# Performance work log

Hardware: AMD Instinct MI355X
Metric: run time of the kernel (lower is better)

Reference implementation:

```python
import jax, jax.numpy as jnp
import numpy as np

WAYS, SHOTS = 5, 5
F_DIM, HID = 1024, 512          # num_node_feats, int(1024*0.5)
BATCH = 2048                    # num_tasks
N = WAYS * SHOTS + 1            # 26 samples per episode
BN_EPS = 1e-5


def setup_inputs() -> dict:
    key = jax.random.key(0)
    ks = jax.random.split(key, 12)
    d = {"node_feats": jax.random.normal(ks[0], (BATCH, N, F_DIM), jnp.float32)}
    # conv1 (1x1): F_DIM -> HID, bn1; conv2: HID -> HID, bn2; conv4: HID -> F_DIM
    d["w1"] = jax.random.normal(ks[1], (HID, F_DIM), jnp.float32) * (1.0 / np.sqrt(F_DIM))
    d["b1"] = jax.random.normal(ks[2], (HID,), jnp.float32) * 0.01
    d["g1"] = jnp.ones((HID,), jnp.float32)
    d["be1"] = jnp.zeros((HID,), jnp.float32)
    d["m1"] = jax.random.normal(ks[3], (HID,), jnp.float32) * 0.1
    d["v1"] = jax.random.uniform(ks[4], (HID,), jnp.float32, 0.5, 1.5)
    d["w2"] = jax.random.normal(ks[5], (HID, HID), jnp.float32) * (1.0 / np.sqrt(HID))
    d["b2"] = jax.random.normal(ks[6], (HID,), jnp.float32) * 0.01
    d["g2"] = jnp.ones((HID,), jnp.float32)
    d["be2"] = jnp.zeros((HID,), jnp.float32)
    d["m2"] = jax.random.normal(ks[7], (HID,), jnp.float32) * 0.1
    d["v2"] = jax.random.uniform(ks[8], (HID,), jnp.float32, 0.5, 1.5)
    d["w3"] = jax.random.normal(ks[9], (F_DIM, HID), jnp.float32) * (1.0 / np.sqrt(HID))
    d["b3"] = jax.random.normal(ks[10], (F_DIM,), jnp.float32) * 0.01
    return d


def _conv1x1(x, w, b):
    # x: [B, Cin, N], w: [Cout, Cin] -> [B, Cout, N]
    return jnp.einsum('bcn,oc->bon', x, w) + b[None, :, None]


def _bn(x, g, be, m, v):
    # inference BatchNorm1d over channel dim of [B, C, N]
    scale = g / jnp.sqrt(v + BN_EPS)
    return (x - m[None, :, None]) * scale[None, :, None] + be[None, :, None]


def _forward(node_feats, w1, b1, g1, be1, m1, v1, w2, b2, g2, be2, m2, v2, w3, b3):
    B, n, F = node_feats.shape  # n == WAYS*SHOTS+1
    # in-place per-class mean on the transpose view also mutates node_feats in torch:
    sup = node_feats[:, :WAYS * SHOTS].reshape(B, WAYS, SHOTS, F)
    sup = jnp.broadcast_to(sup.mean(axis=2, keepdims=True), sup.shape).reshape(B, WAYS * SHOTS, F)
    nf = jnp.concatenate([sup, node_feats[:, WAYS * SHOTS:]], axis=1)  # [B, N, F]

    x = nf.transpose(0, 2, 1)  # [B, F, N]
    x = jax.nn.leaky_relu(_bn(_conv1x1(x, w1, b1), g1, be1, m1, v1), 0.01)
    x = jax.nn.leaky_relu(_bn(_conv1x1(x, w2, b2), g2, be2, m2, v2), 0.01)
    att = jax.nn.sigmoid(_conv1x1(x, w3, b3))  # [B, F, N]

    # sim_cal: cosine sim of u_ij = a_i*a_j*x_i vs v_ij = a_i*a_j*x_j, fused into matmuls.
    a = att.transpose(0, 2, 1)       # [B, N, F]
    a2 = a * a                       # attention squared
    P = a2 * nf                      # dot(u,v)   = (P P^T)[i,j]
    Q = a2 * nf * nf                 # ||u_ij||^2 = (Q a2^T)[i,j]
    dots = jnp.einsum('bif,bjf->bij', P, P)    # [B, N, N]
    n2 = jnp.einsum('bif,bjf->bij', Q, a2)     # [B, N, N]
    nrm = jnp.sqrt(n2)
    sim = dots / (nrm * nrm.transpose(0, 2, 1))
    pred = jnp.stack([sim, 1.0 - sim], axis=1)  # [B, 2, N, N]
    return jnp.clip(pred, 0.0, 1.0)


def reference(node_feats, w1, b1, g1, be1, m1, v1, w2, b2, g2, be2, m2, v2, w3, b3):
    return _forward(node_feats, w1, b1, g1, be1, m1, v1, w2, b2, g2, be2, m2, v2, w3, b3)
```

## Files before the change

kernel.cpp:

```cpp
#include <hip/hip_runtime.h>
#include <hip/hip_bf16.h>
#include <math.h>

typedef __bf16 bf16_t;
typedef bf16_t bf16x8 __attribute__((ext_vector_type(8)));
typedef float f32x4 __attribute__((ext_vector_type(4)));

#define WAYS 5
#define SHOTS 5
#define F_DIM 1024
#define HID 512
#define BATCH 2048
#define NN 26
#define NC 6
#define MROWS (BATCH * NC)

#define S1 (HID * F_DIM)
#define S2 (HID * HID)
#define S3 (F_DIM * HID)

#define TM 48
#define PADX 520

__global__ __launch_bounds__(256)
void cvt_all_kernel(const float* __restrict__ w1, const float* __restrict__ w2,
                    const float* __restrict__ w3, bf16_t* __restrict__ out) {
    int i = (blockIdx.x * 256 + threadIdx.x) * 4;
    if (i >= S1 + S2 + S3) return;
    const float* src;
    int j = i;
    if (i < S1)            { src = w1; }
    else if (i < S1 + S2)  { src = w2; j = i - S1; }
    else                   { src = w3; j = i - S1 - S2; }
    float4 v = *(const float4*)(src + j);
    out[i + 0] = (bf16_t)v.x;
    out[i + 1] = (bf16_t)v.y;
    out[i + 2] = (bf16_t)v.z;
    out[i + 3] = (bf16_t)v.w;
}

__global__ __launch_bounds__(128)
void nfc_kernel(const float* __restrict__ node, bf16_t* __restrict__ nfc_b) {
    int row = blockIdx.x;
    int b = row / NC;
    int w = row - b * NC;
    int f = threadIdx.x * 8;
    const float* src = node + (size_t)b * NN * F_DIM;
    float acc[8];
    if (w < WAYS) {
        #pragma unroll
        for (int e = 0; e < 8; ++e) acc[e] = 0.f;
        #pragma unroll
        for (int s = 0; s < SHOTS; ++s) {
            const float* r = src + (size_t)(w * SHOTS + s) * F_DIM + f;
            float4 v0 = *(const float4*)r;
            float4 v1 = *(const float4*)(r + 4);
            acc[0] += v0.x; acc[1] += v0.y; acc[2] += v0.z; acc[3] += v0.w;
            acc[4] += v1.x; acc[5] += v1.y; acc[6] += v1.z; acc[7] += v1.w;
        }
        #pragma unroll
        for (int e = 0; e < 8; ++e) acc[e] *= 0.2f;
    } else {
        const float* r = src + (size_t)25 * F_DIM + f;
        float4 v0 = *(const float4*)r;
        float4 v1 = *(const float4*)(r + 4);
        acc[0] = v0.x; acc[1] = v0.y; acc[2] = v0.z; acc[3] = v0.w;
        acc[4] = v1.x; acc[5] = v1.y; acc[6] = v1.z; acc[7] = v1.w;
    }
    bf16x8 ob;
    #pragma unroll
    for (int e = 0; e < 8; ++e) ob[e] = (bf16_t)acc[e];
    *(bf16x8*)(nfc_b + (size_t)row * F_DIM + f) = ob;
}

__global__ __launch_bounds__(256)
void fused_mlp(const bf16_t* __restrict__ nfc, const bf16_t* __restrict__ w1b,
               const bf16_t* __restrict__ w2b, const bf16_t* __restrict__ w3b,
               bf16_t* __restrict__ att,
               const float* __restrict__ b1, const float* __restrict__ g1,
               const float* __restrict__ be1, const float* __restrict__ m1,
               const float* __restrict__ v1,
               const float* __restrict__ b2, const float* __restrict__ g2,
               const float* __restrict__ be2, const float* __restrict__ m2,
               const float* __restrict__ v2,
               const float* __restrict__ b3) {
    __shared__ bf16_t X1[TM * PADX];
    __shared__ bf16_t X2[TM * PADX];
    const int tid = threadIdx.x;
    const int lane = tid & 63;
    const int wv = tid >> 6;
    const int l15 = lane & 15, quad = lane >> 4;
    const int bm = blockIdx.x * TM;
    const int nb = wv * 128;

    f32x4 acc[3][8];

    auto mmac = [&](bf16x8 (&af)[6], bf16x8 (&bf)[16]) {
        #pragma unroll
        for (int kk = 0; kk < 2; ++kk)
            #pragma unroll
            for (int mt = 0; mt < 3; ++mt)
                #pragma unroll
                for (int nt = 0; nt < 8; ++nt)
                    acc[mt][nt] = __builtin_amdgcn_mfma_f32_16x16x32_bf16(
                        af[mt * 2 + kk], bf[nt * 2 + kk], acc[mt][nt], 0, 0, 0);
    };
    auto ldB = [&](bf16x8 (&bf)[16], const bf16_t* W, int K, int c) {
        #pragma unroll
        for (int nt = 0; nt < 8; ++nt)
            #pragma unroll
            for (int kk = 0; kk < 2; ++kk)
                bf[nt * 2 + kk] = *(const bf16x8*)(W + (size_t)(nb + nt * 16 + l15) * K
                                                   + c * 64 + kk * 32 + quad * 8);
    };
    auto ldA1 = [&](bf16x8 (&af)[6], int c) {
        #pragma unroll
        for (int mt = 0; mt < 3; ++mt)
            #pragma unroll
            for (int kk = 0; kk < 2; ++kk)
                af[mt * 2 + kk] = *(const bf16x8*)(nfc + (size_t)(bm + mt * 16 + l15) * F_DIM
                                                    + c * 64 + kk * 32 + quad * 8);
    };
    auto ldAx = [&](bf16x8 (&af)[6], int which, int c) {
        #pragma unroll
        for (int mt = 0; mt < 3; ++mt)
            #pragma unroll
            for (int kk = 0; kk < 2; ++kk) {
                int idx = (mt * 16 + l15) * PADX + c * 64 + kk * 32 + quad * 8;
                af[mt * 2 + kk] = which ? *(const bf16x8*)&X2[idx] : *(const bf16x8*)&X1[idx];
            }
    };

    bf16x8 aF0[6], aF1[6], bF0[16], bF1[16];

    #pragma unroll
    for (int mt = 0; mt < 3; ++mt)
        #pragma unroll
        for (int nt = 0; nt < 8; ++nt)
            acc[mt][nt] = (f32x4){0.f, 0.f, 0.f, 0.f};
    ldA1(aF0, 0); ldB(bF0, w1b, F_DIM, 0);
    for (int c = 0; c < 16; c += 2) {
        ldA1(aF1, c + 1); ldB(bF1, w1b, F_DIM, c + 1);
        mmac(aF0, bF0);
        if (c + 2 < 16) { ldA1(aF0, c + 2); ldB(bF0, w1b, F_DIM, c + 2); }
        mmac(aF1, bF1);
    }
    #pragma unroll
    for (int nt = 0; nt < 8; ++nt) {
        const int n = nb + nt * 16 + l15;
        const float sg = g1[n] * rsqrtf(v1[n] + 1e-5f);
        const float tt = (b1[n] - m1[n]) * sg + be1[n];
        #pragma unroll
        for (int mt = 0; mt < 3; ++mt) {
            const int row = mt * 16 + quad * 4;
            #pragma unroll
            for (int r = 0; r < 4; ++r) {
                float y = acc[mt][nt][r] * sg + tt;
                y = y > 0.f ? y : 0.01f * y;
                X1[(row + r) * PADX + n] = (bf16_t)y;
            }
        }
    }
    __syncthreads();

    #pragma unroll
    for (int mt = 0; mt < 3; ++mt)
        #pragma unroll
        for (int nt = 0; nt < 8; ++nt)
            acc[mt][nt] = (f32x4){0.f, 0.f, 0.f, 0.f};
    ldB(bF0, w2b, HID, 0);
    for (int c = 0; c < 8; c += 2) {
        ldB(bF1, w2b, HID, c + 1);
        ldAx(aF0, 0, c);
        mmac(aF0, bF0);
        if (c + 2 < 8) ldB(bF0, w2b, HID, c + 2);
        ldAx(aF1, 0, c + 1);
        mmac(aF1, bF1);
    }
    #pragma unroll
    for (int nt = 0; nt < 8; ++nt) {
        const int n = nb + nt * 16 + l15;
        const float sg = g2[n] * rsqrtf(v2[n] + 1e-5f);
        const float tt = (b2[n] - m2[n]) * sg + be2[n];
        #pragma unroll
        for (int mt = 0; mt < 3; ++mt) {
            const int row = mt * 16 + quad * 4;
            #pragma unroll
            for (int r = 0; r < 4; ++r) {
                float y = acc[mt][nt][r] * sg + tt;
                y = y > 0.f ? y : 0.01f * y;
                X2[(row + r) * PADX + n] = (bf16_t)y;
            }
        }
    }
    __syncthreads();

    #pragma unroll
    for (int h = 0; h < 2; ++h) {
        const bf16_t* w3h = w3b + (size_t)(h * 512) * HID;
        #pragma unroll
        for (int mt = 0; mt < 3; ++mt)
            #pragma unroll
            for (int nt = 0; nt < 8; ++nt)
                acc[mt][nt] = (f32x4){0.f, 0.f, 0.f, 0.f};
        ldB(bF0, w3h, HID, 0);
        for (int c = 0; c < 8; c += 2) {
            ldB(bF1, w3h, HID, c + 1);
            ldAx(aF0, 1, c);
            mmac(aF0, bF0);
            if (c + 2 < 8) ldB(bF0, w3h, HID, c + 2);
            ldAx(aF1, 1, c + 1);
            mmac(aF1, bF1);
        }
        #pragma unroll
        for (int nt = 0; nt < 8; ++nt) {
            const int n = h * 512 + nb + nt * 16 + l15;
            const float tt = b3[n];
            #pragma unroll
            for (int mt = 0; mt < 3; ++mt) {
                const int m = bm + mt * 16 + quad * 4;
                #pragma unroll
                for (int r = 0; r < 4; ++r) {
                    float y = acc[mt][nt][r] + tt;
                    y = 1.0f / (1.0f + __expf(-y));
                    att[(size_t)(m + r) * F_DIM + n] = (bf16_t)y;
                }
            }
        }
    }
}

__global__ __launch_bounds__(256)
void sim_kernel(const bf16_t* __restrict__ nfc, const bf16_t* __restrict__ att,
                float* __restrict__ out) {
    __shared__ float sx[NC * F_DIM];
    __shared__ float sa[NC * F_DIM];
    __shared__ float dmat[NC * NC], n2mat[NC * NC], simc[NC * NC];
    const int b = blockIdx.x, tid = threadIdx.x;
    const bf16_t* xs = nfc + (size_t)b * NC * F_DIM;
    const bf16_t* as = att + (size_t)b * NC * F_DIM;
    for (int i = tid * 8; i < NC * F_DIM; i += 256 * 8) {
        bf16x8 vx = *(const bf16x8*)&xs[i];
        bf16x8 va = *(const bf16x8*)&as[i];
        #pragma unroll
        for (int e = 0; e < 8; ++e) { sx[i + e] = (float)vx[e]; sa[i + e] = (float)va[e]; }
    }
    __syncthreads();
    const int lane = tid & 63, wid = tid >> 6;
    const int ti[21] = {0,0,0,0,0,0,1,1,1,1,1,2,2,2,2,3,3,3,4,4,5};
    const int tj[21] = {0,1,2,3,4,5,1,2,3,4,5,2,3,4,5,3,4,5,4,5,5};
    for (int t = wid; t < 21; t += 4) {
        const int i = ti[t], j = tj[t];
        float d = 0.f, qij = 0.f, qji = 0.f;
        for (int f = lane; f < F_DIM; f += 64) {
            float ai = sa[i * F_DIM + f], aj = sa[j * F_DIM + f];
            float xi = sx[i * F_DIM + f], xj = sx[j * F_DIM + f];
            float a2i = ai * ai, a2j = aj * aj;
            float pi = a2i * xi, pj = a2j * xj;
            d   += pi * pj;
            qij += pi * xi * a2j;
            qji += pj * xj * a2i;
        }
        #pragma unroll
        for (int off = 32; off > 0; off >>= 1) {
            d   += __shfl_xor(d, off);
            qij += __shfl_xor(qij, off);
            qji += __shfl_xor(qji, off);
        }
        if (lane == 0) {
            dmat[i * NC + j] = d; dmat[j * NC + i] = d;
            n2mat[i * NC + j] = qij; n2mat[j * NC + i] = qji;
        }
    }
    __syncthreads();
    if (tid < NC * NC) {
        int i = tid / NC, j = tid - (tid / NC) * NC;
        simc[tid] = dmat[tid] / sqrtf(n2mat[i * NC + j] * n2mat[j * NC + i]);
    }
    __syncthreads();
    float* o = out + (size_t)b * (2 * NN * NN);
    for (int e = tid; e < 2 * NN * NN; e += 256) {
        int ch = e / (NN * NN);
        int rem = e - ch * (NN * NN);
        int i = rem / NN, j = rem - (rem / NN) * NN;
        float s = simc[(i / 5) * NC + (j / 5)];
        float v = ch ? 1.0f - s : s;
        v = fminf(fmaxf(v, 0.0f), 1.0f);
        o[e] = v;
    }
}

extern "C" void kernel_launch(void* const* d_in, const int* in_sizes, int n_in,
                              void* d_out, int out_size, void* d_ws, size_t ws_size,
                              hipStream_t stream) {
    const float* node = (const float*)d_in[0];
    const float* w1  = (const float*)d_in[1];
    const float* b1  = (const float*)d_in[2];
    const float* g1  = (const float*)d_in[3];
    const float* be1 = (const float*)d_in[4];
    const float* m1  = (const float*)d_in[5];
    const float* v1  = (const float*)d_in[6];
    const float* w2  = (const float*)d_in[7];
    const float* b2  = (const float*)d_in[8];
    const float* g2  = (const float*)d_in[9];
    const float* be2 = (const float*)d_in[10];
    const float* m2  = (const float*)d_in[11];
    const float* v2  = (const float*)d_in[12];
    const float* w3  = (const float*)d_in[13];
    const float* b3  = (const float*)d_in[14];
    float* out = (float*)d_out;

    char* ws = (char*)d_ws;
    size_t off = 0;
    bf16_t* wall  = (bf16_t*)(ws + off); off += (size_t)(S1 + S2 + S3) * 2;
    bf16_t* w1b = wall, *w2b = wall + S1, *w3b = wall + S1 + S2;
    bf16_t* nfc_b = (bf16_t*)(ws + off); off += (size_t)MROWS * F_DIM * 2;
    bf16_t* attb  = (bf16_t*)(ws + off); off += (size_t)MROWS * F_DIM * 2;

    cvt_all_kernel<<<((S1 + S2 + S3) / 4 + 255) / 256, 256, 0, stream>>>(w1, w2, w3, wall);
    nfc_kernel<<<MROWS, 128, 0, stream>>>(node, nfc_b);
    fused_mlp<<<MROWS / TM, 256, 0, stream>>>(nfc_b, w1b, w2b, w3b, attb,
                                              b1, g1, be1, m1, v1,
                                              b2, g2, be2, m2, v2, b3);
    sim_kernel<<<BATCH, 256, 0, stream>>>(nfc_b, attb, out);
}
```

Baseline: 468.4 us.

## Split fused MLP across eight waves with smaller per-wave N tiles

Doubles the fused_mlp block from 256 to 512 threads, so each of eight waves covers 64 output columns instead of 128. This halves the accumulator and B-fragment registers per wave and adds a launch-bounds hint of two blocks per CU, aiming for more resident waves to hide memory latency. It also software-pipelines the LDS A-fragment loads in layers 2 and 3 alongside the B loads. In exchange, each W row is fetched by twice as many waves relative to the MFMA work, and the 2x~50KB LDS footprint may limit how many blocks actually fit.

```diff
diff --git a/kernel.cpp b/kernel.cpp
--- a/kernel.cpp
+++ b/kernel.cpp
@@ -73,7 +73,7 @@
     *(bf16x8*)(nfc_b + (size_t)row * F_DIM + f) = ob;
 }
 
-__global__ __launch_bounds__(256)
+__global__ __launch_bounds__(512, 2)
 void fused_mlp(const bf16_t* __restrict__ nfc, const bf16_t* __restrict__ w1b,
                const bf16_t* __restrict__ w2b, const bf16_t* __restrict__ w3b,
                bf16_t* __restrict__ att,
@@ -91,23 +91,30 @@
     const int wv = tid >> 6;
     const int l15 = lane & 15, quad = lane >> 4;
     const int bm = blockIdx.x * TM;
-    const int nb = wv * 128;
-
-    f32x4 acc[3][8];
-
-    auto mmac = [&](bf16x8 (&af)[6], bf16x8 (&bf)[16]) {
+    const int nb = wv * 64;
+
+    f32x4 acc[3][4];
+
+    auto mmac = [&](bf16x8 (&af)[6], bf16x8 (&bf)[8]) {
         #pragma unroll
         for (int kk = 0; kk < 2; ++kk)
             #pragma unroll
             for (int mt = 0; mt < 3; ++mt)
                 #pragma unroll
-                for (int nt = 0; nt < 8; ++nt)
+                for (int nt = 0; nt < 4; ++nt)
                     acc[mt][nt] = __builtin_amdgcn_mfma_f32_16x16x32_bf16(
                         af[mt * 2 + kk], bf[nt * 2 + kk], acc[mt][nt], 0, 0, 0);
     };
-    auto ldB = [&](bf16x8 (&bf)[16], const bf16_t* W, int K, int c) {
-        #pragma unroll
-        for (int nt = 0; nt < 8; ++nt)
+    auto zacc = [&]() {
+        #pragma unroll
+        for (int mt = 0; mt < 3; ++mt)
+            #pragma unroll
+            for (int nt = 0; nt < 4; ++nt)
+                acc[mt][nt] = (f32x4){0.f, 0.f, 0.f, 0.f};
+    };
+    auto ldB = [&](bf16x8 (&bf)[8], const bf16_t* W, int K, int c) {
+        #pragma unroll
+        for (int nt = 0; nt < 4; ++nt)
             #pragma unroll
             for (int kk = 0; kk < 2; ++kk)
                 bf[nt * 2 + kk] = *(const bf16x8*)(W + (size_t)(nb + nt * 16 + l15) * K
@@ -131,13 +138,9 @@
             }
     };
 
-    bf16x8 aF0[6], aF1[6], bF0[16], bF1[16];
-
-    #pragma unroll
-    for (int mt = 0; mt < 3; ++mt)
-        #pragma unroll
-        for (int nt = 0; nt < 8; ++nt)
-            acc[mt][nt] = (f32x4){0.f, 0.f, 0.f, 0.f};
+    bf16x8 aF0[6], aF1[6], bF0[8], bF1[8];
+
+    zacc();
     ldA1(aF0, 0); ldB(bF0, w1b, F_DIM, 0);
     for (int c = 0; c < 16; c += 2) {
         ldA1(aF1, c + 1); ldB(bF1, w1b, F_DIM, c + 1);
@@ -146,7 +149,7 @@
         mmac(aF1, bF1);
     }
     #pragma unroll
-    for (int nt = 0; nt < 8; ++nt) {
+    for (int nt = 0; nt < 4; ++nt) {
         const int n = nb + nt * 16 + l15;
         const float sg = g1[n] * rsqrtf(v1[n] + 1e-5f);
         const float tt = (b1[n] - m1[n]) * sg + be1[n];
@@ -163,22 +166,16 @@
     }
     __syncthreads();
 
+    zacc();
+    ldAx(aF0, 0, 0); ldB(bF0, w2b, HID, 0);
+    for (int c = 0; c < 8; c += 2) {
+        ldAx(aF1, 0, c + 1); ldB(bF1, w2b, HID, c + 1);
+        mmac(aF0, bF0);
+        if (c + 2 < 8) { ldAx(aF0, 0, c + 2); ldB(bF0, w2b, HID, c + 2); }
+        mmac(aF1, bF1);
+    }
     #pragma unroll
-    for (int mt = 0; mt < 3; ++mt)
-        #pragma unroll
-        for (int nt = 0; nt < 8; ++nt)
-            acc[mt][nt] = (f32x4){0.f, 0.f, 0.f, 0.f};
-    ldB(bF0, w2b, HID, 0);
-    for (int c = 0; c < 8; c += 2) {
-        ldB(bF1, w2b, HID, c + 1);
-        ldAx(aF0, 0, c);
-        mmac(aF0, bF0);
-        if (c + 2 < 8) ldB(bF0, w2b, HID, c + 2);
-        ldAx(aF1, 0, c + 1);
-        mmac(aF1, bF1);
-    }
-    #pragma unroll
-    for (int nt = 0; nt < 8; ++nt) {
+    for (int nt = 0; nt < 4; ++nt) {
         const int n = nb + nt * 16 + l15;
         const float sg = g2[n] * rsqrtf(v2[n] + 1e-5f);
         const float tt = (b2[n] - m2[n]) * sg + be2[n];
@@ -198,22 +195,16 @@
     #pragma unroll
     for (int h = 0; h < 2; ++h) {
         const bf16_t* w3h = w3b + (size_t)(h * 512) * HID;
-        #pragma unroll
-        for (int mt = 0; mt < 3; ++mt)
-            #pragma unroll
-            for (int nt = 0; nt < 8; ++nt)
-                acc[mt][nt] = (f32x4){0.f, 0.f, 0.f, 0.f};
-        ldB(bF0, w3h, HID, 0);
+        zacc();
+        ldAx(aF0, 1, 0); ldB(bF0, w3h, HID, 0);
         for (int c = 0; c < 8; c += 2) {
-            ldB(bF1, w3h, HID, c + 1);
-            ldAx(aF0, 1, c);
+            ldAx(aF1, 1, c + 1); ldB(bF1, w3h, HID, c + 1);
             mmac(aF0, bF0);
-            if (c + 2 < 8) ldB(bF0, w3h, HID, c + 2);
-            ldAx(aF1, 1, c + 1);
+            if (c + 2 < 8) { ldAx(aF0, 1, c + 2); ldB(bF0, w3h, HID, c + 2); }
             mmac(aF1, bF1);
         }
         #pragma unroll
-        for (int nt = 0; nt < 8; ++nt) {
+        for (int nt = 0; nt < 4; ++nt) {
             const int n = h * 512 + nb + nt * 16 + l15;
             const float tt = b3[n];
             #pragma unroll
@@ -319,7 +310,7 @@
 
     cvt_all_kernel<<<((S1 + S2 + S3) / 4 + 255) / 256, 256, 0, stream>>>(w1, w2, w3, wall);
     nfc_kernel<<<MROWS, 128, 0, stream>>>(node, nfc_b);
-    fused_mlp<<<MROWS / TM, 256, 0, stream>>>(nfc_b, w1b, w2b, w3b, attb,
+    fused_mlp<<<MROWS / TM, 512, 0, stream>>>(nfc_b, w1b, w2b, w3b, attb,
                                               b1, g1, be1, m1, v1,
                                               b2, g2, be2, m2, v2, b3);
     sim_kernel<<<BATCH, 256, 0, stream>>>(nfc_b, attb, out);
```

Measured after the change: 465.8 us. Within noise of the previous version (-0.6%).
